# Kernel optimization log

Measured on AMD Instinct MI355X. Metric: run time of the kernel, lower is better.

The kernel has to match this reference:

```python
import jax, jax.numpy as jnp
import numpy as np

EPS = 1e-7  # keras backend epsilon


def setup_inputs() -> dict:
    key = jax.random.key(0)
    k1, k2, k3, k4, k5 = jax.random.split(key, 5)
    B, L, D, U = 8, 1024, 256, 256
    seq_data = jax.random.normal(k1, (B, L, D), dtype=jnp.float32)
    graph = jax.random.uniform(k2, (B, L, L), dtype=jnp.float32)
    scale = 1.0 / np.sqrt(D)
    e_weight = jax.random.normal(k3, (D, U), dtype=jnp.float32) * scale
    Wx = jax.random.normal(k4, (U, U), dtype=jnp.float32) * scale
    Wh = jax.random.normal(k5, (U, U), dtype=jnp.float32) * scale
    b = jnp.zeros((U,), dtype=jnp.float32)
    return {"seq_data": seq_data, "graph": graph, "e_weight": e_weight,
            "Wx": Wx, "Wh": Wh, "b": b}


def reference(seq_data, graph, e_weight, Wx, Wh, b):
    # beta = seq_data @ e_weight : (B, L, U)
    beta = jnp.einsum('bld,du->blu', seq_data, e_weight)
    # normalize_graph_output: divide by out-degree sum over axis 2 -> (B, L)
    norm = jnp.maximum(jnp.sum(graph, axis=2), EPS)
    beta = beta / norm[:, :, None]
    # K.batch_dot(beta(B,L,U), graph(B,L,M), axes=(1,1)) -> (B,U,M), then
    # permute (0,2,1) -> (B,M,U); fused as a single einsum.
    agg = jnp.einsum('blu,blm->bmu', beta, graph)  # (B, L, U)
    B, L, U = agg.shape
    h0 = jnp.zeros((B, U), dtype=agg.dtype)  # get_initial_state: zeros

    def step(h, x):  # SimpleRNNCell: h' = tanh(x Wx + h Wh + b)
        h = jnp.tanh(x @ Wx + h @ Wh + b)
        return h, h

    _, ys = jax.lax.scan(step, h0, jnp.swapaxes(agg, 0, 1))  # (L, B, U)
    return jnp.swapaxes(ys, 0, 1)  # (B, L, U)
```

## Files before the change

kernel.cpp:

```cpp
#include <hip/hip_runtime.h>
#include <hip/hip_bf16.h>


typedef unsigned short u16;
typedef unsigned int u32;
typedef __bf16 bf16_t;
typedef __bf16 bf16x8 __attribute__((ext_vector_type(8)));
typedef float f32x4 __attribute__((ext_vector_type(4)));
typedef unsigned short u16x8 __attribute__((ext_vector_type(8)));
typedef unsigned short u16x4 __attribute__((ext_vector_type(4)));

#define LDS_P 72
#define HP_B  288

struct HiLo { u16 hi, lo; };

__device__ __forceinline__ u16 f2bf(float f) {
  bf16_t h = (bf16_t)f;
  return __builtin_bit_cast(u16, h);
}
__device__ __forceinline__ HiLo splitf(float v) {
  bf16_t h = (bf16_t)v;
  HiLo r;
  r.hi = __builtin_bit_cast(u16, h);
  r.lo = f2bf(v - (float)h);
  return r;
}
__device__ __forceinline__ float tanh_fast(float x) {
  float ax = fabsf(x);
  float e  = __expf(-2.0f * ax);
  float t  = __fdividef(1.0f - e, 1.0f + e);
  return copysignf(t, x);
}
__device__ __forceinline__ void sync_lds_only() {
  __asm__ volatile("s_waitcnt lgkmcnt(0)\ns_barrier" ::: "memory");
}

__global__ void prep_split_rowsum(const float* __restrict__ E, u16* __restrict__ Eth, u16* __restrict__ Etl,
                                  const float* __restrict__ Wx, u16* __restrict__ Wxth, u16* __restrict__ Wxtl,
                                  const float* __restrict__ Wh, u16* __restrict__ Whth, u16* __restrict__ Whtl,
                                  const float* __restrict__ graph, float* __restrict__ rnorm) {
  const int bid = blockIdx.x;
  if (bid < 768) {
    const int mat = bid >> 8, u = bid & 255, d = threadIdx.x;
    const float* s; u16 *dh, *dl;
    if (mat == 0)      { s = E;  dh = Eth;  dl = Etl; }
    else if (mat == 1) { s = Wx; dh = Wxth; dl = Wxtl; }
    else               { s = Wh; dh = Whth; dl = Whtl; }
    HiLo r = splitf(s[d * 256 + u]);
    dh[u * 256 + d] = r.hi;
    dl[u * 256 + d] = r.lo;
  } else {
    const int wave = threadIdx.x >> 6, lane = threadIdx.x & 63;
    const int row = (bid - 768) * 4 + wave;
    const float* p = graph + (size_t)row * 1024 + lane * 16;
    float s = 0.f;
#pragma unroll
    for (int c = 0; c < 4; c++) {
      f32x4 v = *(const f32x4*)(p + c * 4);
#pragma unroll
      for (int j = 0; j < 4; j++) s += v[j];
    }
#pragma unroll
    for (int off = 32; off > 0; off >>= 1) s += __shfl_xor(s, off);
    if (lane == 0) rnorm[row] = 1.0f / fmaxf(s, 1e-7f);
  }
}

__global__ __launch_bounds__(256, 2) void gemm_beta(const float* __restrict__ seq,
                                                    const u16* __restrict__ Eth,
                                                    const u16* __restrict__ Etl,
                                                    const float* __restrict__ rnorm,
                                                    u16* __restrict__ betaTh,
                                                    u16* __restrict__ betaTl) {
  __shared__ u16 Ah[64 * LDS_P], Al[64 * LDS_P];
  __shared__ u16 Bh[64 * LDS_P], Bl[64 * LDS_P];
  const int t = threadIdx.x;
  const int wave = t >> 6, lane = t & 63, quad = lane >> 4, l16 = lane & 15;
  const int r0 = blockIdx.x * 64, n0 = blockIdx.y * 64;
  f32x4 acc[4];
#pragma unroll
  for (int i = 0; i < 4; i++) acc[i] = (f32x4){0.f, 0.f, 0.f, 0.f};

  for (int kb = 0; kb < 256; kb += 64) {
#pragma unroll
    for (int cc = 0; cc < 4; cc++) {
      int c = t + cc * 256;
      int r = c >> 4, c4 = c & 15;
      f32x4 v = *(const f32x4*)(seq + (size_t)(r0 + r) * 256 + kb + c4 * 4);
      u16x4 hi, lo;
#pragma unroll
      for (int j = 0; j < 4; j++) {
        HiLo s = splitf(v[j]);
        hi[j] = s.hi; lo[j] = s.lo;
      }
      *(u16x4*)(Ah + r * LDS_P + c4 * 4) = hi;
      *(u16x4*)(Al + r * LDS_P + c4 * 4) = lo;
    }
#pragma unroll
    for (int cc = 0; cc < 2; cc++) {
      int c = t + cc * 256;
      int r = c >> 3, c8 = c & 7;
      *(u16x8*)(Bh + r * LDS_P + c8 * 8) =
          *(const u16x8*)(Eth + (size_t)(n0 + r) * 256 + kb + c8 * 8);
      *(u16x8*)(Bl + r * LDS_P + c8 * 8) =
          *(const u16x8*)(Etl + (size_t)(n0 + r) * 256 + kb + c8 * 8);
    }
    __syncthreads();
#pragma unroll
    for (int kk = 0; kk < 64; kk += 32) {
      bf16x8 ah = __builtin_bit_cast(bf16x8, *(const u16x8*)(Ah + (wave * 16 + l16) * LDS_P + kk + quad * 8));
      bf16x8 al = __builtin_bit_cast(bf16x8, *(const u16x8*)(Al + (wave * 16 + l16) * LDS_P + kk + quad * 8));
#pragma unroll
      for (int tN = 0; tN < 4; tN++) {
        bf16x8 bh = __builtin_bit_cast(bf16x8, *(const u16x8*)(Bh + (tN * 16 + l16) * LDS_P + kk + quad * 8));
        bf16x8 bl = __builtin_bit_cast(bf16x8, *(const u16x8*)(Bl + (tN * 16 + l16) * LDS_P + kk + quad * 8));
        acc[tN] = __builtin_amdgcn_mfma_f32_16x16x32_bf16(ah, bh, acc[tN], 0, 0, 0);
        acc[tN] = __builtin_amdgcn_mfma_f32_16x16x32_bf16(ah, bl, acc[tN], 0, 0, 0);
        acc[tN] = __builtin_amdgcn_mfma_f32_16x16x32_bf16(al, bh, acc[tN], 0, 0, 0);
      }
    }
    __syncthreads();
  }
  const int rbase = r0 + wave * 16 + quad * 4;
  float rn[4];
#pragma unroll
  for (int i = 0; i < 4; i++) rn[i] = rnorm[rbase + i];
  const int bI = rbase >> 10, lI = rbase & 1023;
#pragma unroll
  for (int tN = 0; tN < 4; tN++) {
    int u = n0 + tN * 16 + l16;
    u16x4 hv, lv;
#pragma unroll
    for (int i = 0; i < 4; i++) {
      HiLo s = splitf(acc[tN][i] * rn[i]);
      hv[i] = s.hi; lv[i] = s.lo;
    }
    size_t off = ((size_t)bI << 18) + (size_t)u * 1024 + lI;
    *(u16x4*)(betaTh + off) = hv;
    *(u16x4*)(betaTl + off) = lv;
  }
}

__global__ __launch_bounds__(256, 2) void gemm_agg(const float* __restrict__ graph,
                                                   const u16* __restrict__ betaTh,
                                                   const u16* __restrict__ betaTl,
                                                   float* __restrict__ agg) {
  __shared__ u16 Ah[64 * LDS_P], Al[64 * LDS_P];
  __shared__ u16 Bh[64 * LDS_P], Bl[64 * LDS_P];
  const int t = threadIdx.x;
  const int wave = t >> 6, lane = t & 63, quad = lane >> 4, l16 = lane & 15;
  const int m0 = blockIdx.x * 64, n0 = blockIdx.y * 64, b = blockIdx.z;
  const float* g = graph + (size_t)b * (1024 * 1024);
  const size_t bt = (size_t)b << 18;
  f32x4 acc[4];
#pragma unroll
  for (int i = 0; i < 4; i++) acc[i] = (f32x4){0.f, 0.f, 0.f, 0.f};

  for (int kb = 0; kb < 1024; kb += 64) {
#pragma unroll
    for (int cc = 0; cc < 4; cc++) {
      int c = t + cc * 256;
      int r = c >> 4, c4 = c & 15;
      f32x4 v = *(const f32x4*)(g + (size_t)(kb + r) * 1024 + m0 + c4 * 4);
#pragma unroll
      for (int j = 0; j < 4; j++) {
        HiLo s = splitf(v[j]);
        Ah[(c4 * 4 + j) * LDS_P + r] = s.hi;
        Al[(c4 * 4 + j) * LDS_P + r] = s.lo;
      }
    }
#pragma unroll
    for (int cc = 0; cc < 2; cc++) {
      int c = t + cc * 256;
      int r = c >> 3, c8 = c & 7;
      *(u16x8*)(Bh + r * LDS_P + c8 * 8) =
          *(const u16x8*)(betaTh + bt + (size_t)(n0 + r) * 1024 + kb + c8 * 8);
      *(u16x8*)(Bl + r * LDS_P + c8 * 8) =
          *(const u16x8*)(betaTl + bt + (size_t)(n0 + r) * 1024 + kb + c8 * 8);
    }
    __syncthreads();
#pragma unroll
    for (int kk = 0; kk < 64; kk += 32) {
      bf16x8 ah = __builtin_bit_cast(bf16x8, *(const u16x8*)(Ah + (wave * 16 + l16) * LDS_P + kk + quad * 8));
      bf16x8 al = __builtin_bit_cast(bf16x8, *(const u16x8*)(Al + (wave * 16 + l16) * LDS_P + kk + quad * 8));
#pragma unroll
      for (int tN = 0; tN < 4; tN++) {
        bf16x8 bh = __builtin_bit_cast(bf16x8, *(const u16x8*)(Bh + (tN * 16 + l16) * LDS_P + kk + quad * 8));
        bf16x8 bl = __builtin_bit_cast(bf16x8, *(const u16x8*)(Bl + (tN * 16 + l16) * LDS_P + kk + quad * 8));
        acc[tN] = __builtin_amdgcn_mfma_f32_16x16x32_bf16(ah, bh, acc[tN], 0, 0, 0);
        acc[tN] = __builtin_amdgcn_mfma_f32_16x16x32_bf16(ah, bl, acc[tN], 0, 0, 0);
        acc[tN] = __builtin_amdgcn_mfma_f32_16x16x32_bf16(al, bh, acc[tN], 0, 0, 0);
      }
    }
    __syncthreads();
  }
  const int mbase = m0 + wave * 16 + quad * 4;
#pragma unroll
  for (int tN = 0; tN < 4; tN++) {
    int u = n0 + tN * 16 + l16;
#pragma unroll
    for (int i = 0; i < 4; i++)
      agg[((size_t)b * 1024 + mbase + i) * 256 + u] = acc[tN][i];
  }
}

__global__ __launch_bounds__(256, 2) void gemm_xpre(const float* __restrict__ agg,
                                                    const u16* __restrict__ Wxth,
                                                    const u16* __restrict__ Wxtl,
                                                    const float* __restrict__ bias,
                                                    float* __restrict__ Xpre) {
  __shared__ u16 Ah[64 * LDS_P], Al[64 * LDS_P];
  __shared__ u16 Bh[64 * LDS_P], Bl[64 * LDS_P];
  const int t = threadIdx.x;
  const int wave = t >> 6, lane = t & 63, quad = lane >> 4, l16 = lane & 15;
  const int r0 = blockIdx.x * 64, n0 = blockIdx.y * 64;
  f32x4 acc[4];
#pragma unroll
  for (int i = 0; i < 4; i++) acc[i] = (f32x4){0.f, 0.f, 0.f, 0.f};

  for (int kb = 0; kb < 256; kb += 64) {
#pragma unroll
    for (int cc = 0; cc < 4; cc++) {
      int c = t + cc * 256;
      int r = c >> 4, c4 = c & 15;
      f32x4 v = *(const f32x4*)(agg + (size_t)(r0 + r) * 256 + kb + c4 * 4);
      u16x4 hi, lo;
#pragma unroll
      for (int j = 0; j < 4; j++) {
        HiLo s = splitf(v[j]);
        hi[j] = s.hi; lo[j] = s.lo;
      }
      *(u16x4*)(Ah + r * LDS_P + c4 * 4) = hi;
      *(u16x4*)(Al + r * LDS_P + c4 * 4) = lo;
    }
#pragma unroll
    for (int cc = 0; cc < 2; cc++) {
      int c = t + cc * 256;
      int r = c >> 3, c8 = c & 7;
      *(u16x8*)(Bh + r * LDS_P + c8 * 8) =
          *(const u16x8*)(Wxth + (size_t)(n0 + r) * 256 + kb + c8 * 8);
      *(u16x8*)(Bl + r * LDS_P + c8 * 8) =
          *(const u16x8*)(Wxtl + (size_t)(n0 + r) * 256 + kb + c8 * 8);
    }
    __syncthreads();
#pragma unroll
    for (int kk = 0; kk < 64; kk += 32) {
      bf16x8 ah = __builtin_bit_cast(bf16x8, *(const u16x8*)(Ah + (wave * 16 + l16) * LDS_P + kk + quad * 8));
      bf16x8 al = __builtin_bit_cast(bf16x8, *(const u16x8*)(Al + (wave * 16 + l16) * LDS_P + kk + quad * 8));
#pragma unroll
      for (int tN = 0; tN < 4; tN++) {
        bf16x8 bh = __builtin_bit_cast(bf16x8, *(const u16x8*)(Bh + (tN * 16 + l16) * LDS_P + kk + quad * 8));
        bf16x8 bl = __builtin_bit_cast(bf16x8, *(const u16x8*)(Bl + (tN * 16 + l16) * LDS_P + kk + quad * 8));
        acc[tN] = __builtin_amdgcn_mfma_f32_16x16x32_bf16(ah, bh, acc[tN], 0, 0, 0);
        acc[tN] = __builtin_amdgcn_mfma_f32_16x16x32_bf16(ah, bl, acc[tN], 0, 0, 0);
        acc[tN] = __builtin_amdgcn_mfma_f32_16x16x32_bf16(al, bh, acc[tN], 0, 0, 0);
      }
    }
    __syncthreads();
  }
  const int rbase = r0 + wave * 16 + quad * 4;
  const int bI = rbase >> 10;
#pragma unroll
  for (int tN = 0; tN < 4; tN++) {
    int u = n0 + tN * 16 + l16;
    float bu = bias[u];
#pragma unroll
    for (int i = 0; i < 4; i++) {
      int mI = (rbase + i) & 1023;
      Xpre[((size_t)mI * 8 + bI) * 256 + u] = acc[tN][i] + bu;
    }
  }
}

__global__ __launch_bounds__(512, 2) void rnn_scan(const u16* __restrict__ Whth,
                                                   const u16* __restrict__ Whtl,
                                                   const float* __restrict__ Xpre,
                                                   float* __restrict__ out) {
  __shared__ u16 h2[2][2 * HP_B];
  const int b = blockIdx.x;
  const int t = threadIdx.x;
  const int w = t >> 6, lane = t & 63, quad = lane >> 4, l16 = lane & 15;
  const int colbase = w * 32;
  const bool epi = (quad < 2);
  const int col_e = colbase + quad * 16 + l16;

  bf16x8 bwh[2][8], bwl[2][8];
#pragma unroll
  for (int tN = 0; tN < 2; tN++) {
    const u16* wph = Whth + (size_t)(colbase + tN * 16 + l16) * 256 + quad * 8;
    const u16* wpl = Whtl + (size_t)(colbase + tN * 16 + l16) * 256 + quad * 8;
#pragma unroll
    for (int kb = 0; kb < 8; kb++) {
      bwh[tN][kb] = __builtin_bit_cast(bf16x8, *(const u16x8*)(wph + kb * 32));
      bwl[tN][kb] = __builtin_bit_cast(bf16x8, *(const u16x8*)(wpl + kb * 32));
    }
  }
  for (int i = t; i < 2 * 2 * HP_B; i += 512) ((u16*)h2)[i] = 0;

  float cb[4];
  if (epi) {
#pragma unroll
    for (int k = 0; k < 4; k++) cb[k] = Xpre[(size_t)k * 2048 + b * 256 + col_e];
  }
  const float* ldp = Xpre + 4 * 2048 + b * 256 + col_e;
  float* outp = out + (size_t)b * 262144 + col_e;
  const u16* rb0 = &h2[0][(l16 & 1) * HP_B + quad * 8];
  const u16* rb1 = &h2[1][(l16 & 1) * HP_B + quad * 8];
  u16* wb0 = &h2[0][0];
  u16* wb1 = &h2[1][0];
  __syncthreads();

  for (int m4 = 0; m4 < 1024; m4 += 4) {
#pragma unroll
    for (int k = 0; k < 4; k++) {
      const int p = k & 1;
      const u16* rb = p ? rb1 : rb0;
      u16* hw = p ? wb0 : wb1;

      bf16x8 af[8];
#pragma unroll
      for (int kb = 0; kb < 8; kb++)
        af[kb] = __builtin_bit_cast(bf16x8, *(const u16x8*)(rb + kb * 32));

      f32x4 a0a = {0.f,0.f,0.f,0.f}, a0b = {0.f,0.f,0.f,0.f};
      f32x4 a1a = {0.f,0.f,0.f,0.f}, a1b = {0.f,0.f,0.f,0.f};
#pragma unroll
      for (int kb = 0; kb < 4; kb++) {
        a0a = __builtin_amdgcn_mfma_f32_16x16x32_bf16(af[kb], bwh[0][kb], a0a, 0, 0, 0);
        a1a = __builtin_amdgcn_mfma_f32_16x16x32_bf16(af[kb], bwh[1][kb], a1a, 0, 0, 0);
        a0b = __builtin_amdgcn_mfma_f32_16x16x32_bf16(af[kb + 4], bwh[0][kb + 4], a0b, 0, 0, 0);
        a1b = __builtin_amdgcn_mfma_f32_16x16x32_bf16(af[kb + 4], bwh[1][kb + 4], a1b, 0, 0, 0);
        a0a = __builtin_amdgcn_mfma_f32_16x16x32_bf16(af[kb], bwl[0][kb], a0a, 0, 0, 0);
        a1a = __builtin_amdgcn_mfma_f32_16x16x32_bf16(af[kb], bwl[1][kb], a1a, 0, 0, 0);
        a0b = __builtin_amdgcn_mfma_f32_16x16x32_bf16(af[kb + 4], bwl[0][kb + 4], a0b, 0, 0, 0);
        a1b = __builtin_amdgcn_mfma_f32_16x16x32_bf16(af[kb + 4], bwl[1][kb + 4], a1b, 0, 0, 0);
      }

      if (epi) {
        float sA0 = quad ? a1a[0] : a0a[0];
        float sA1 = quad ? a1a[1] : a0a[1];
        float sB0 = quad ? a1b[0] : a0b[0];
        float sB1 = quad ? a1b[1] : a0b[1];
        float hi_part = sA0 + sB0;
        float lo_part = sA1 + sB1;
        float x = (hi_part + lo_part) + cb[k];
        float y = tanh_fast(x);
        HiLo s = splitf(y);
        hw[col_e] = s.hi;
        hw[HP_B + col_e] = s.lo;
        *outp = y;
        if (m4 <= 1019 - k) {
          cb[k] = *ldp;
          ldp += 2048;
        }
      }
      outp += 256;
      sync_lds_only();
    }
  }
}

extern "C" void kernel_launch(void* const* d_in, const int* in_sizes, int n_in,
                              void* d_out, int out_size, void* d_ws, size_t ws_size,
                              hipStream_t stream) {
  (void)in_sizes; (void)n_in; (void)out_size; (void)ws_size;
  const float* seq   = (const float*)d_in[0];
  const float* graph = (const float*)d_in[1];
  const float* E     = (const float*)d_in[2];
  const float* Wx    = (const float*)d_in[3];
  const float* Wh    = (const float*)d_in[4];
  const float* bias  = (const float*)d_in[5];
  float* out = (float*)d_out;

  char* w = (char*)d_ws;
  float* rnorm  = (float*)(w + 0);
  u16*   Eth    = (u16*)(w + 32768);
  u16*   Etl    = (u16*)(w + 163840);
  u16*   Wxth   = (u16*)(w + 294912);
  u16*   Wxtl   = (u16*)(w + 425984);
  u16*   Whth   = (u16*)(w + 557056);
  u16*   Whtl   = (u16*)(w + 688128);
  u16*   betaTh = (u16*)(w + 819200);
  u16*   betaTl = (u16*)(w + 5013504);
  float* agg    = (float*)(w + 9207808);
  float* Xpre   = (float*)(w + 17596416);

  prep_split_rowsum<<<2816, 256, 0, stream>>>(E, Eth, Etl, Wx, Wxth, Wxtl, Wh, Whth, Whtl, graph, rnorm);
  gemm_beta<<<dim3(128, 4), 256, 0, stream>>>(seq, Eth, Etl, rnorm, betaTh, betaTl);
  gemm_agg<<<dim3(16, 4, 8), 256, 0, stream>>>(graph, betaTh, betaTl, agg);
  gemm_xpre<<<dim3(128, 4), 256, 0, stream>>>(agg, Wxth, Wxtl, bias, Xpre);
  rnn_scan<<<dim3(8), 512, 0, stream>>>(Whth, Whtl, Xpre, out);
}
```

Baseline: 777.5 us.

## Fuse front GEMM stages into cooperative kernel and defer RNN output stores

```diff
diff --git a/kernel.cpp b/kernel.cpp
--- a/kernel.cpp
+++ b/kernel.cpp
@@ -1,5 +1,7 @@
 #include <hip/hip_runtime.h>
 #include <hip/hip_bf16.h>
+#include <hip/hip_cooperative_groups.h>
+namespace cg = cooperative_groups;
 
 
 typedef unsigned short u16;
@@ -36,13 +38,14 @@
   __asm__ volatile("s_waitcnt lgkmcnt(0)\ns_barrier" ::: "memory");
 }
 
-__global__ void prep_split_rowsum(const float* __restrict__ E, u16* __restrict__ Eth, u16* __restrict__ Etl,
-                                  const float* __restrict__ Wx, u16* __restrict__ Wxth, u16* __restrict__ Wxtl,
-                                  const float* __restrict__ Wh, u16* __restrict__ Whth, u16* __restrict__ Whtl,
-                                  const float* __restrict__ graph, float* __restrict__ rnorm) {
-  const int bid = blockIdx.x;
-  if (bid < 768) {
-    const int mat = bid >> 8, u = bid & 255, d = threadIdx.x;
+
+__device__ __forceinline__ void prep_body(int v, int tid,
+    const float* __restrict__ E, u16* __restrict__ Eth, u16* __restrict__ Etl,
+    const float* __restrict__ Wx, u16* __restrict__ Wxth, u16* __restrict__ Wxtl,
+    const float* __restrict__ Wh, u16* __restrict__ Whth, u16* __restrict__ Whtl,
+    const float* __restrict__ graph, float* __restrict__ rnorm) {
+  if (v < 768) {
+    const int mat = v >> 8, u = v & 255, d = tid;
     const float* s; u16 *dh, *dl;
     if (mat == 0)      { s = E;  dh = Eth;  dl = Etl; }
     else if (mat == 1) { s = Wx; dh = Wxth; dl = Wxtl; }
@@ -51,15 +54,15 @@
     dh[u * 256 + d] = r.hi;
     dl[u * 256 + d] = r.lo;
   } else {
-    const int wave = threadIdx.x >> 6, lane = threadIdx.x & 63;
-    const int row = (bid - 768) * 4 + wave;
+    const int wave = tid >> 6, lane = tid & 63;
+    const int row = (v - 768) * 4 + wave;
     const float* p = graph + (size_t)row * 1024 + lane * 16;
     float s = 0.f;
 #pragma unroll
     for (int c = 0; c < 4; c++) {
-      f32x4 v = *(const f32x4*)(p + c * 4);
-#pragma unroll
-      for (int j = 0; j < 4; j++) s += v[j];
+      f32x4 vv = *(const f32x4*)(p + c * 4);
+#pragma unroll
+      for (int j = 0; j < 4; j++) s += vv[j];
     }
 #pragma unroll
     for (int off = 32; off > 0; off >>= 1) s += __shfl_xor(s, off);
@@ -67,17 +70,13 @@
   }
 }
 
-__global__ __launch_bounds__(256, 2) void gemm_beta(const float* __restrict__ seq,
-                                                    const u16* __restrict__ Eth,
-                                                    const u16* __restrict__ Etl,
-                                                    const float* __restrict__ rnorm,
-                                                    u16* __restrict__ betaTh,
-                                                    u16* __restrict__ betaTl) {
-  __shared__ u16 Ah[64 * LDS_P], Al[64 * LDS_P];
-  __shared__ u16 Bh[64 * LDS_P], Bl[64 * LDS_P];
-  const int t = threadIdx.x;
+__device__ __forceinline__ void beta_body(int v, int t,
+    const float* __restrict__ seq, const u16* __restrict__ Eth,
+    const u16* __restrict__ Etl, const float* __restrict__ rnorm,
+    u16* __restrict__ betaTh, u16* __restrict__ betaTl,
+    u16* Ah, u16* Al, u16* Bh, u16* Bl) {
   const int wave = t >> 6, lane = t & 63, quad = lane >> 4, l16 = lane & 15;
-  const int r0 = blockIdx.x * 64, n0 = blockIdx.y * 64;
+  const int r0 = (v >> 2) * 64, n0 = (v & 3) * 64;
   f32x4 acc[4];
 #pragma unroll
   for (int i = 0; i < 4; i++) acc[i] = (f32x4){0.f, 0.f, 0.f, 0.f};
@@ -87,11 +86,11 @@
     for (int cc = 0; cc < 4; cc++) {
       int c = t + cc * 256;
       int r = c >> 4, c4 = c & 15;
-      f32x4 v = *(const f32x4*)(seq + (size_t)(r0 + r) * 256 + kb + c4 * 4);
+      f32x4 vv = *(const f32x4*)(seq + (size_t)(r0 + r) * 256 + kb + c4 * 4);
       u16x4 hi, lo;
 #pragma unroll
       for (int j = 0; j < 4; j++) {
-        HiLo s = splitf(v[j]);
+        HiLo s = splitf(vv[j]);
         hi[j] = s.hi; lo[j] = s.lo;
       }
       *(u16x4*)(Ah + r * LDS_P + c4 * 4) = hi;
@@ -142,15 +141,12 @@
   }
 }
 
-__global__ __launch_bounds__(256, 2) void gemm_agg(const float* __restrict__ graph,
-                                                   const u16* __restrict__ betaTh,
-                                                   const u16* __restrict__ betaTl,
-                                                   float* __restrict__ agg) {
-  __shared__ u16 Ah[64 * LDS_P], Al[64 * LDS_P];
-  __shared__ u16 Bh[64 * LDS_P], Bl[64 * LDS_P];
-  const int t = threadIdx.x;
+__device__ __forceinline__ void agg_body(int v, int t,
+    const float* __restrict__ graph, const u16* __restrict__ betaTh,
+    const u16* __restrict__ betaTl, float* __restrict__ agg,
+    u16* Ah, u16* Al, u16* Bh, u16* Bl) {
   const int wave = t >> 6, lane = t & 63, quad = lane >> 4, l16 = lane & 15;
-  const int m0 = blockIdx.x * 64, n0 = blockIdx.y * 64, b = blockIdx.z;
+  const int m0 = (v & 15) * 64, n0 = ((v >> 4) & 3) * 64, b = v >> 6;
   const float* g = graph + (size_t)b * (1024 * 1024);
   const size_t bt = (size_t)b << 18;
   f32x4 acc[4];
@@ -162,10 +158,10 @@
     for (int cc = 0; cc < 4; cc++) {
       int c = t + cc * 256;
       int r = c >> 4, c4 = c & 15;
-      f32x4 v = *(const f32x4*)(g + (size_t)(kb + r) * 1024 + m0 + c4 * 4);
+      f32x4 vv = *(const f32x4*)(g + (size_t)(kb + r) * 1024 + m0 + c4 * 4);
 #pragma unroll
       for (int j = 0; j < 4; j++) {
-        HiLo s = splitf(v[j]);
+        HiLo s = splitf(vv[j]);
         Ah[(c4 * 4 + j) * LDS_P + r] = s.hi;
         Al[(c4 * 4 + j) * LDS_P + r] = s.lo;
       }
@@ -205,16 +201,13 @@
   }
 }
 
-__global__ __launch_bounds__(256, 2) void gemm_xpre(const float* __restrict__ agg,
-                                                    const u16* __restrict__ Wxth,
-                                                    const u16* __restrict__ Wxtl,
-                                                    const float* __restrict__ bias,
-                                                    float* __restrict__ Xpre) {
-  __shared__ u16 Ah[64 * LDS_P], Al[64 * LDS_P];
-  __shared__ u16 Bh[64 * LDS_P], Bl[64 * LDS_P];
-  const int t = threadIdx.x;
+__device__ __forceinline__ void xpre_body(int v, int t,
+    const float* __restrict__ agg, const u16* __restrict__ Wxth,
+    const u16* __restrict__ Wxtl, const float* __restrict__ bias,
+    float* __restrict__ Xpre,
+    u16* Ah, u16* Al, u16* Bh, u16* Bl) {
   const int wave = t >> 6, lane = t & 63, quad = lane >> 4, l16 = lane & 15;
-  const int r0 = blockIdx.x * 64, n0 = blockIdx.y * 64;
+  const int r0 = (v >> 2) * 64, n0 = (v & 3) * 64;
   f32x4 acc[4];
 #pragma unroll
   for (int i = 0; i < 4; i++) acc[i] = (f32x4){0.f, 0.f, 0.f, 0.f};
@@ -224,11 +217,11 @@
     for (int cc = 0; cc < 4; cc++) {
       int c = t + cc * 256;
       int r = c >> 4, c4 = c & 15;
-      f32x4 v = *(const f32x4*)(agg + (size_t)(r0 + r) * 256 + kb + c4 * 4);
+      f32x4 vv = *(const f32x4*)(agg + (size_t)(r0 + r) * 256 + kb + c4 * 4);
       u16x4 hi, lo;
 #pragma unroll
       for (int j = 0; j < 4; j++) {
-        HiLo s = splitf(v[j]);
+        HiLo s = splitf(vv[j]);
         hi[j] = s.hi; lo[j] = s.lo;
       }
       *(u16x4*)(Ah + r * LDS_P + c4 * 4) = hi;
@@ -271,6 +264,46 @@
       Xpre[((size_t)mI * 8 + bI) * 256 + u] = acc[tN][i] + bu;
     }
   }
+}
+
+__global__ void k_prep(const float* E, u16* Eth, u16* Etl,
+                       const float* Wx, u16* Wxth, u16* Wxtl,
+                       const float* Wh, u16* Whth, u16* Whtl,
+                       const float* graph, float* rnorm) {
+  prep_body(blockIdx.x, threadIdx.x, E, Eth, Etl, Wx, Wxth, Wxtl, Wh, Whth, Whtl, graph, rnorm);
+}
+__global__ __launch_bounds__(256, 2) void k_beta(const float* seq, const u16* Eth, const u16* Etl,
+                                                 const float* rnorm, u16* betaTh, u16* betaTl) {
+  __shared__ u16 Ah[64 * LDS_P], Al[64 * LDS_P], Bh[64 * LDS_P], Bl[64 * LDS_P];
+  beta_body(blockIdx.x, threadIdx.x, seq, Eth, Etl, rnorm, betaTh, betaTl, Ah, Al, Bh, Bl);
+}
+__global__ __launch_bounds__(256, 2) void k_agg(const float* graph, const u16* betaTh, const u16* betaTl,
+                                                float* agg) {
+  __shared__ u16 Ah[64 * LDS_P], Al[64 * LDS_P], Bh[64 * LDS_P], Bl[64 * LDS_P];
+  agg_body(blockIdx.x, threadIdx.x, graph, betaTh, betaTl, agg, Ah, Al, Bh, Bl);
+}
+__global__ __launch_bounds__(256, 2) void k_xpre(const float* agg, const u16* Wxth, const u16* Wxtl,
+                                                 const float* bias, float* Xpre) {
+  __shared__ u16 Ah[64 * LDS_P], Al[64 * LDS_P], Bh[64 * LDS_P], Bl[64 * LDS_P];
+  xpre_body(blockIdx.x, threadIdx.x, agg, Wxth, Wxtl, bias, Xpre, Ah, Al, Bh, Bl);
+}
+
+__global__ __launch_bounds__(256, 2) void fused_front(
+    const float* seq, const float* graph, const float* E, const float* Wx,
+    const float* Wh, const float* bias,
+    u16* Eth, u16* Etl, u16* Wxth, u16* Wxtl, u16* Whth, u16* Whtl,
+    float* rnorm, u16* betaTh, u16* betaTl, float* agg, float* Xpre) {
+  __shared__ u16 Ah[64 * LDS_P], Al[64 * LDS_P], Bh[64 * LDS_P], Bl[64 * LDS_P];
+  cg::grid_group grid = cg::this_grid();
+  const int t = threadIdx.x;
+  for (int v = blockIdx.x; v < 2816; v += 512)
+    prep_body(v, t, E, Eth, Etl, Wx, Wxth, Wxtl, Wh, Whth, Whtl, graph, rnorm);
+  grid.sync();
+  beta_body(blockIdx.x, t, seq, Eth, Etl, rnorm, betaTh, betaTl, Ah, Al, Bh, Bl);
+  grid.sync();
+  agg_body(blockIdx.x, t, graph, betaTh, betaTl, agg, Ah, Al, Bh, Bl);
+  grid.sync();
+  xpre_body(blockIdx.x, t, agg, Wxth, Wxtl, bias, Xpre, Ah, Al, Bh, Bl);
 }
 
 __global__ __launch_bounds__(512, 2) void rnn_scan(const u16* __restrict__ Whth,
@@ -305,6 +338,7 @@
   }
   const float* ldp = Xpre + 4 * 2048 + b * 256 + col_e;
   float* outp = out + (size_t)b * 262144 + col_e;
+  float y_prev = 0.f;
   const u16* rb0 = &h2[0][(l16 & 1) * HP_B + quad * 8];
   const u16* rb1 = &h2[1][(l16 & 1) * HP_B + quad * 8];
   u16* wb0 = &h2[0][0];
@@ -322,6 +356,11 @@
 #pragma unroll
       for (int kb = 0; kb < 8; kb++)
         af[kb] = __builtin_bit_cast(bf16x8, *(const u16x8*)(rb + kb * 32));
+
+      if (epi) {
+        if (m4 + k > 0) { *outp = y_prev; outp += 256; }
+        if (m4 + k >= 1 && m4 + k <= 1020) { cb[(k + 3) & 3] = *ldp; ldp += 2048; }
+      }
 
       f32x4 a0a = {0.f,0.f,0.f,0.f}, a0b = {0.f,0.f,0.f,0.f};
       f32x4 a1a = {0.f,0.f,0.f,0.f}, a1b = {0.f,0.f,0.f,0.f};
@@ -349,16 +388,12 @@
         HiLo s = splitf(y);
         hw[col_e] = s.hi;
         hw[HP_B + col_e] = s.lo;
-        *outp = y;
-        if (m4 <= 1019 - k) {
-          cb[k] = *ldp;
-          ldp += 2048;
-        }
-      }
-      outp += 256;
+        y_prev = y;
+      }
       sync_lds_only();
     }
   }
+  if (epi) *outp = y_prev;
 }
 
 extern "C" void kernel_launch(void* const* d_in, const int* in_sizes, int n_in,
@@ -386,9 +421,16 @@
   float* agg    = (float*)(w + 9207808);
   float* Xpre   = (float*)(w + 17596416);
 
-  prep_split_rowsum<<<2816, 256, 0, stream>>>(E, Eth, Etl, Wx, Wxth, Wxtl, Wh, Whth, Whtl, graph, rnorm);
-  gemm_beta<<<dim3(128, 4), 256, 0, stream>>>(seq, Eth, Etl, rnorm, betaTh, betaTl);
-  gemm_agg<<<dim3(16, 4, 8), 256, 0, stream>>>(graph, betaTh, betaTl, agg);
-  gemm_xpre<<<dim3(128, 4), 256, 0, stream>>>(agg, Wxth, Wxtl, bias, Xpre);
+  void* args[] = {&seq, &graph, &E, &Wx, &Wh, &bias,
+                  &Eth, &Etl, &Wxth, &Wxtl, &Whth, &Whtl,
+                  &rnorm, &betaTh, &betaTl, &agg, &Xpre};
+  hipError_t ce = hipLaunchCooperativeKernel((void*)fused_front, dim3(512), dim3(256),
+                                             args, 0, stream);
+  if (ce != hipSuccess) {
+    k_prep<<<2816, 256, 0, stream>>>(E, Eth, Etl, Wx, Wxth, Wxtl, Wh, Whth, Whtl, graph, rnorm);
+    k_beta<<<512, 256, 0, stream>>>(seq, Eth, Etl, rnorm, betaTh, betaTl);
+    k_agg<<<512, 256, 0, stream>>>(graph, betaTh, betaTl, agg);
+    k_xpre<<<512, 256, 0, stream>>>(agg, Wxth, Wxtl, bias, Xpre);
+  }
   rnn_scan<<<dim3(8), 512, 0, stream>>>(Whth, Whtl, Xpre, out);
 }
```

Result: slower. 1.025 ms (+31.8%).

## Merge prep and beta GEMM into one launch, apply row norm in agg

Applied to the files above, without the earlier changes.

```diff
diff --git a/kernel.cpp b/kernel.cpp
--- a/kernel.cpp
+++ b/kernel.cpp
@@ -36,23 +36,30 @@
   __asm__ volatile("s_waitcnt lgkmcnt(0)\ns_barrier" ::: "memory");
 }
 
-__global__ void prep_split_rowsum(const float* __restrict__ E, u16* __restrict__ Eth, u16* __restrict__ Etl,
-                                  const float* __restrict__ Wx, u16* __restrict__ Wxth, u16* __restrict__ Wxtl,
-                                  const float* __restrict__ Wh, u16* __restrict__ Whth, u16* __restrict__ Whtl,
-                                  const float* __restrict__ graph, float* __restrict__ rnorm) {
+__global__ __launch_bounds__(256, 2) void front1(
+    const float* __restrict__ Wx, u16* __restrict__ Wxth, u16* __restrict__ Wxtl,
+    const float* __restrict__ Wh, u16* __restrict__ Whth, u16* __restrict__ Whtl,
+    const float* __restrict__ graph, float* __restrict__ rnorm,
+    const float* __restrict__ seq, const float* __restrict__ E,
+    u16* __restrict__ betaTh, u16* __restrict__ betaTl) {
+  __shared__ u16 Ah[64 * LDS_P], Al[64 * LDS_P];
+  __shared__ u16 Bh[64 * LDS_P], Bl[64 * LDS_P];
   const int bid = blockIdx.x;
-  if (bid < 768) {
-    const int mat = bid >> 8, u = bid & 255, d = threadIdx.x;
+  const int t = threadIdx.x;
+
+  if (bid < 512) {
+    const int u = bid & 255, d = t;
     const float* s; u16 *dh, *dl;
-    if (mat == 0)      { s = E;  dh = Eth;  dl = Etl; }
-    else if (mat == 1) { s = Wx; dh = Wxth; dl = Wxtl; }
-    else               { s = Wh; dh = Whth; dl = Whtl; }
+    if (bid < 256) { s = Wx; dh = Wxth; dl = Wxtl; }
+    else           { s = Wh; dh = Whth; dl = Whtl; }
     HiLo r = splitf(s[d * 256 + u]);
     dh[u * 256 + d] = r.hi;
     dl[u * 256 + d] = r.lo;
-  } else {
-    const int wave = threadIdx.x >> 6, lane = threadIdx.x & 63;
-    const int row = (bid - 768) * 4 + wave;
+    return;
+  }
+  if (bid < 2560) {
+    const int wave = t >> 6, lane = t & 63;
+    const int row = (bid - 512) * 4 + wave;
     const float* p = graph + (size_t)row * 1024 + lane * 16;
     float s = 0.f;
 #pragma unroll
@@ -64,20 +71,12 @@
 #pragma unroll
     for (int off = 32; off > 0; off >>= 1) s += __shfl_xor(s, off);
     if (lane == 0) rnorm[row] = 1.0f / fmaxf(s, 1e-7f);
-  }
-}
-
-__global__ __launch_bounds__(256, 2) void gemm_beta(const float* __restrict__ seq,
-                                                    const u16* __restrict__ Eth,
-                                                    const u16* __restrict__ Etl,
-                                                    const float* __restrict__ rnorm,
-                                                    u16* __restrict__ betaTh,
-                                                    u16* __restrict__ betaTl) {
-  __shared__ u16 Ah[64 * LDS_P], Al[64 * LDS_P];
-  __shared__ u16 Bh[64 * LDS_P], Bl[64 * LDS_P];
-  const int t = threadIdx.x;
+    return;
+  }
+
+  const int v = bid - 2560;
   const int wave = t >> 6, lane = t & 63, quad = lane >> 4, l16 = lane & 15;
-  const int r0 = blockIdx.x * 64, n0 = blockIdx.y * 64;
+  const int n0 = (v & 3) * 64, r0 = (v >> 2) * 64;
   f32x4 acc[4];
 #pragma unroll
   for (int i = 0; i < 4; i++) acc[i] = (f32x4){0.f, 0.f, 0.f, 0.f};
@@ -87,24 +86,27 @@
     for (int cc = 0; cc < 4; cc++) {
       int c = t + cc * 256;
       int r = c >> 4, c4 = c & 15;
-      f32x4 v = *(const f32x4*)(seq + (size_t)(r0 + r) * 256 + kb + c4 * 4);
+      f32x4 vv = *(const f32x4*)(seq + (size_t)(r0 + r) * 256 + kb + c4 * 4);
       u16x4 hi, lo;
 #pragma unroll
       for (int j = 0; j < 4; j++) {
-        HiLo s = splitf(v[j]);
+        HiLo s = splitf(vv[j]);
         hi[j] = s.hi; lo[j] = s.lo;
       }
       *(u16x4*)(Ah + r * LDS_P + c4 * 4) = hi;
       *(u16x4*)(Al + r * LDS_P + c4 * 4) = lo;
     }
 #pragma unroll
-    for (int cc = 0; cc < 2; cc++) {
-      int c = t + cc * 256;
-      int r = c >> 3, c8 = c & 7;
-      *(u16x8*)(Bh + r * LDS_P + c8 * 8) =
-          *(const u16x8*)(Eth + (size_t)(n0 + r) * 256 + kb + c8 * 8);
-      *(u16x8*)(Bl + r * LDS_P + c8 * 8) =
-          *(const u16x8*)(Etl + (size_t)(n0 + r) * 256 + kb + c8 * 8);
+    for (int cc = 0; cc < 4; cc++) {
+      int c = t + cc * 256;
+      int r = c >> 4, c4 = c & 15;
+      f32x4 vv = *(const f32x4*)(E + (size_t)(kb + r) * 256 + n0 + c4 * 4);
+#pragma unroll
+      for (int j = 0; j < 4; j++) {
+        HiLo s = splitf(vv[j]);
+        Bh[(c4 * 4 + j) * LDS_P + r] = s.hi;
+        Bl[(c4 * 4 + j) * LDS_P + r] = s.lo;
+      }
     }
     __syncthreads();
 #pragma unroll
@@ -123,9 +125,6 @@
     __syncthreads();
   }
   const int rbase = r0 + wave * 16 + quad * 4;
-  float rn[4];
-#pragma unroll
-  for (int i = 0; i < 4; i++) rn[i] = rnorm[rbase + i];
   const int bI = rbase >> 10, lI = rbase & 1023;
 #pragma unroll
   for (int tN = 0; tN < 4; tN++) {
@@ -133,7 +132,7 @@
     u16x4 hv, lv;
 #pragma unroll
     for (int i = 0; i < 4; i++) {
-      HiLo s = splitf(acc[tN][i] * rn[i]);
+      HiLo s = splitf(acc[tN][i]);
       hv[i] = s.hi; lv[i] = s.lo;
     }
     size_t off = ((size_t)bI << 18) + (size_t)u * 1024 + lI;
@@ -145,6 +144,7 @@
 __global__ __launch_bounds__(256, 2) void gemm_agg(const float* __restrict__ graph,
                                                    const u16* __restrict__ betaTh,
                                                    const u16* __restrict__ betaTl,
+                                                   const float* __restrict__ rnorm,
                                                    float* __restrict__ agg) {
   __shared__ u16 Ah[64 * LDS_P], Al[64 * LDS_P];
   __shared__ u16 Bh[64 * LDS_P], Bl[64 * LDS_P];
@@ -152,6 +152,7 @@
   const int wave = t >> 6, lane = t & 63, quad = lane >> 4, l16 = lane & 15;
   const int m0 = blockIdx.x * 64, n0 = blockIdx.y * 64, b = blockIdx.z;
   const float* g = graph + (size_t)b * (1024 * 1024);
+  const float* rnb = rnorm + b * 1024;
   const size_t bt = (size_t)b << 18;
   f32x4 acc[4];
 #pragma unroll
@@ -163,9 +164,10 @@
       int c = t + cc * 256;
       int r = c >> 4, c4 = c & 15;
       f32x4 v = *(const f32x4*)(g + (size_t)(kb + r) * 1024 + m0 + c4 * 4);
+      float rn = rnb[kb + r];
 #pragma unroll
       for (int j = 0; j < 4; j++) {
-        HiLo s = splitf(v[j]);
+        HiLo s = splitf(v[j] * rn);
         Ah[(c4 * 4 + j) * LDS_P + r] = s.hi;
         Al[(c4 * 4 + j) * LDS_P + r] = s.lo;
       }
@@ -375,8 +377,6 @@
 
   char* w = (char*)d_ws;
   float* rnorm  = (float*)(w + 0);
-  u16*   Eth    = (u16*)(w + 32768);
-  u16*   Etl    = (u16*)(w + 163840);
   u16*   Wxth   = (u16*)(w + 294912);
   u16*   Wxtl   = (u16*)(w + 425984);
   u16*   Whth   = (u16*)(w + 557056);
@@ -386,9 +386,9 @@
   float* agg    = (float*)(w + 9207808);
   float* Xpre   = (float*)(w + 17596416);
 
-  prep_split_rowsum<<<2816, 256, 0, stream>>>(E, Eth, Etl, Wx, Wxth, Wxtl, Wh, Whth, Whtl, graph, rnorm);
-  gemm_beta<<<dim3(128, 4), 256, 0, stream>>>(seq, Eth, Etl, rnorm, betaTh, betaTl);
-  gemm_agg<<<dim3(16, 4, 8), 256, 0, stream>>>(graph, betaTh, betaTl, agg);
+  front1<<<3072, 256, 0, stream>>>(Wx, Wxth, Wxtl, Wh, Whth, Whtl,
+                                   graph, rnorm, seq, E, betaTh, betaTl);
+  gemm_agg<<<dim3(16, 4, 8), 256, 0, stream>>>(graph, betaTh, betaTl, rnorm, agg);
   gemm_xpre<<<dim3(128, 4), 256, 0, stream>>>(agg, Wxth, Wxtl, bias, Xpre);
   rnn_scan<<<dim3(8), 512, 0, stream>>>(Whth, Whtl, Xpre, out);
 }
```

Result: no change. 789.2 us (+1.5%).
